# Kernel tuning notes

Measured on AMD Instinct MI355X. Metric: run time of the kernel, lower is better.

Reference implementation:

```python
import jax, jax.numpy as jnp
import numpy as np

T = 4096
VOCAB = 32000
BLANK = 0


def setup_inputs() -> dict:
    key = jax.random.key(0)
    emission = jax.random.normal(key, (T, VOCAB), dtype=jnp.float32)
    return {"emission": emission}


def reference(emission):
    """Greedy CTC decode: argmax over labels, collapse repeats, drop blanks.

    The torch module returns a variable-length Python list; for a jit-able
    fixed-shape reference we return (padded_indices, count):
      padded_indices: int32 [T], decoded labels left-packed, padded with -1
      count:          int32 scalar, number of valid labels
    """
    idx = jnp.argmax(emission, axis=-1)                      # [T] int
    # unique_consecutive: keep first element of each run
    first_of_run = jnp.concatenate(
        [jnp.array([True]), idx[1:] != idx[:-1]])            # [T] bool
    keep = first_of_run & (idx != BLANK)                     # blank filter
    # stream-compaction: left-pack kept indices, pad with -1
    pos = jnp.cumsum(keep.astype(jnp.int32)) - 1             # [T]
    dest = jnp.where(keep, pos, T)                           # T = out of bounds
    padded = jnp.full((T,), -1, dtype=jnp.int32)
    padded = padded.at[dest].set(idx.astype(jnp.int32), mode="drop")
    count = keep.sum().astype(jnp.int32)
    return padded, count
```

## Files before the change

### kernel.cpp

```cpp
#include <hip/hip_runtime.h>
#include <math.h>

#define T_STEPS 4096
#define VOCAB   32000
#define NV4     (VOCAB / 4)

__device__ __forceinline__ void comb(float& m, int& g, float om, int og) {
    if (om > m || (om == m && og < g)) { m = om; g = og; }
}

__device__ __forceinline__ void upd_group(float& m, int& g, float4 a, int j) {
    const float ma = fmaxf(fmaxf(a.x, a.y), fmaxf(a.z, a.w));
    if (ma > m) { m = ma; g = j; }
}

__global__ __launch_bounds__(256, 8) void ctc_argmax_kernel(const float* __restrict__ em,
                                                            int* __restrict__ idx_out) {
    const int t   = blockIdx.x;
    const int tid = threadIdx.x;
    const float4* row4 = (const float4*)(em + (size_t)t * VOCAB);

    float m0 = -INFINITY, m1 = -INFINITY, m2 = -INFINITY, m3 = -INFINITY;
    int   g0 = 0x7fffffff, g1 = 0x7fffffff, g2 = 0x7fffffff, g3 = 0x7fffffff;

    #pragma unroll 1
    for (int it = 0; it < 7; ++it) {
        const int j = tid + it * 1024;
        const float4 a = row4[j];
        const float4 b = row4[j + 256];
        const float4 c = row4[j + 512];
        const float4 d = row4[j + 768];
        upd_group(m0, g0, a, j);
        upd_group(m1, g1, b, j + 256);
        upd_group(m2, g2, c, j + 512);
        upd_group(m3, g3, d, j + 768);
    }
    {
        const float4 a = row4[7168 + tid];
        upd_group(m0, g0, a, 7168 + tid);
        const float4 b = row4[7424 + tid];
        upd_group(m1, g1, b, 7424 + tid);
        const float4 c = row4[7680 + tid];
        upd_group(m2, g2, c, 7680 + tid);
        if (tid < 64) {
            const float4 d = row4[7936 + tid];
            upd_group(m3, g3, d, 7936 + tid);
        }
    }

    comb(m0, g0, m1, g1);
    comb(m2, g2, m3, g3);
    comb(m0, g0, m2, g2);

    #pragma unroll
    for (int off = 32; off > 0; off >>= 1) {
        const float om = __shfl_down(m0, off, 64);
        const int   og = __shfl_down(g0, off, 64);
        comb(m0, g0, om, og);
    }

    __shared__ float sm[4];
    __shared__ int   sg[4];
    const int lane = tid & 63;
    const int wave = tid >> 6;
    if (lane == 0) { sm[wave] = m0; sg[wave] = g0; }
    __syncthreads();
    if (tid == 0) {
        #pragma unroll
        for (int w = 1; w < 4; ++w) comb(m0, g0, sm[w], sg[w]);
        const float4 win = row4[g0];
        const int c = (win.x == m0) ? 0 : (win.y == m0) ? 1 : (win.z == m0) ? 2 : 3;
        idx_out[t] = g0 * 4 + c;
    }
}

__global__ __launch_bounds__(1024) void ctc_compact_kernel(const int* __restrict__ idx,
                                                           int* __restrict__ out) {
    __shared__ int wsum[16];
    const int tid  = threadIdx.x;
    const int base = tid * 4;

    int v[4], keep[4];
    const int prev0 = (base == 0) ? -1 : idx[base - 1];
    int cnt = 0;
    #pragma unroll
    for (int k = 0; k < 4; ++k) {
        v[k] = idx[base + k];
        const int p = (k == 0) ? prev0 : v[k - 1];
        keep[k] = (v[k] != p && v[k] != 0) ? 1 : 0;
        cnt += keep[k];
    }

    const int lane = tid & 63;
    const int wave = tid >> 6;
    int incl = cnt;
    #pragma unroll
    for (int off = 1; off < 64; off <<= 1) {
        int n = __shfl_up(incl, off, 64);
        if (lane >= off) incl += n;
    }
    if (lane == 63) wsum[wave] = incl;

    #pragma unroll
    for (int k = 0; k < 4; ++k) out[base + k] = -1;
    __syncthreads();

    if (wave == 0) {
        int s = (lane < 16) ? wsum[lane] : 0;
        #pragma unroll
        for (int off = 1; off < 16; off <<= 1) {
            int n = __shfl_up(s, off, 64);
            if (lane >= off) s += n;
        }
        if (lane < 16) wsum[lane] = s;
    }
    __syncthreads();

    const int waveoff = (wave == 0) ? 0 : wsum[wave - 1];
    int pos = waveoff + incl - cnt;
    #pragma unroll
    for (int k = 0; k < 4; ++k) {
        if (keep[k]) out[pos++] = v[k];
    }
    if (tid == 0) out[T_STEPS] = wsum[15];
}

extern "C" void kernel_launch(void* const* d_in, const int* in_sizes, int n_in,
                              void* d_out, int out_size, void* d_ws, size_t ws_size,
                              hipStream_t stream) {
    const float* em  = (const float*)d_in[0];
    int*         out = (int*)d_out;
    int*         idx = (int*)d_ws;

    ctc_argmax_kernel<<<dim3(T_STEPS), dim3(256), 0, stream>>>(em, idx);
    ctc_compact_kernel<<<dim3(1), dim3(1024), 0, stream>>>(idx, out);
}
```

Baseline: 661.1 us.

## Software-pipeline argmax row loads with 8-deep nontemporal register ring

Replaces the 7-iteration loop, which held four independent max accumulators, with a fully unrolled rotating ring of eight in-flight vector loads per thread feeding a single accumulator. The loads use nontemporal hints, and the launch bounds drop from 8 to 4 blocks per SM. The aim is to keep more memory requests in flight per thread and avoid polluting the cache with streaming data. In exchange, the larger register footprint lowers occupancy, and the single accumulator creates a serial compare chain. Because the chunks are visited in increasing order, the tie-breaking still picks the lowest index.

After: 626.2 us. -5.3%, faster.

```diff
diff --git a/kernel.cpp b/kernel.cpp
--- a/kernel.cpp
+++ b/kernel.cpp
@@ -5,72 +5,67 @@
 #define VOCAB   32000
 #define NV4     (VOCAB / 4)
 
+typedef float f32x4 __attribute__((ext_vector_type(4)));
+
 __device__ __forceinline__ void comb(float& m, int& g, float om, int og) {
     if (om > m || (om == m && og < g)) { m = om; g = og; }
 }
 
-__device__ __forceinline__ void upd_group(float& m, int& g, float4 a, int j) {
+__device__ __forceinline__ void upd_group(float& m, int& g, f32x4 a, int j) {
     const float ma = fmaxf(fmaxf(a.x, a.y), fmaxf(a.z, a.w));
     if (ma > m) { m = ma; g = j; }
 }
 
-__global__ __launch_bounds__(256, 8) void ctc_argmax_kernel(const float* __restrict__ em,
+#define NT_LOAD(k) __builtin_nontemporal_load(row4 + tid + (k) * 256)
+#define STEP(vv, it, nxt)                          \
+    upd_group(m, g, vv, tid + (it) * 256);         \
+    if ((nxt) < 31) vv = NT_LOAD(nxt);
+
+__global__ __launch_bounds__(256, 4) void ctc_argmax_kernel(const float* __restrict__ em,
                                                             int* __restrict__ idx_out) {
     const int t   = blockIdx.x;
     const int tid = threadIdx.x;
-    const float4* row4 = (const float4*)(em + (size_t)t * VOCAB);
+    const f32x4* row4 = (const f32x4*)(em + (size_t)t * VOCAB);
 
-    float m0 = -INFINITY, m1 = -INFINITY, m2 = -INFINITY, m3 = -INFINITY;
-    int   g0 = 0x7fffffff, g1 = 0x7fffffff, g2 = 0x7fffffff, g3 = 0x7fffffff;
+    float m = -INFINITY;
+    int   g = 0x7fffffff;
 
-    #pragma unroll 1
-    for (int it = 0; it < 7; ++it) {
-        const int j = tid + it * 1024;
-        const float4 a = row4[j];
-        const float4 b = row4[j + 256];
-        const float4 c = row4[j + 512];
-        const float4 d = row4[j + 768];
-        upd_group(m0, g0, a, j);
-        upd_group(m1, g1, b, j + 256);
-        upd_group(m2, g2, c, j + 512);
-        upd_group(m3, g3, d, j + 768);
+    f32x4 v0 = NT_LOAD(0), v1 = NT_LOAD(1), v2 = NT_LOAD(2), v3 = NT_LOAD(3);
+    f32x4 v4 = NT_LOAD(4), v5 = NT_LOAD(5), v6 = NT_LOAD(6), v7 = NT_LOAD(7);
+
+    STEP(v0,  0,  8) STEP(v1,  1,  9) STEP(v2,  2, 10) STEP(v3,  3, 11)
+    STEP(v4,  4, 12) STEP(v5,  5, 13) STEP(v6,  6, 14) STEP(v7,  7, 15)
+    STEP(v0,  8, 16) STEP(v1,  9, 17) STEP(v2, 10, 18) STEP(v3, 11, 19)
+    STEP(v4, 12, 20) STEP(v5, 13, 21) STEP(v6, 14, 22) STEP(v7, 15, 23)
+    STEP(v0, 16, 24) STEP(v1, 17, 25) STEP(v2, 18, 26) STEP(v3, 19, 27)
+    STEP(v4, 20, 28) STEP(v5, 21, 29) STEP(v6, 22, 30) STEP(v7, 23, 31)
+    STEP(v0, 24, 99) STEP(v1, 25, 99) STEP(v2, 26, 99) STEP(v3, 27, 99)
+    STEP(v4, 28, 99) STEP(v5, 29, 99) STEP(v6, 30, 99)
+
+    if (tid < 64) {
+        const f32x4 tv = __builtin_nontemporal_load(row4 + 7936 + tid);
+        upd_group(m, g, tv, 7936 + tid);
     }
-    {
-        const float4 a = row4[7168 + tid];
-        upd_group(m0, g0, a, 7168 + tid);
-        const float4 b = row4[7424 + tid];
-        upd_group(m1, g1, b, 7424 + tid);
-        const float4 c = row4[7680 + tid];
-        upd_group(m2, g2, c, 7680 + tid);
-        if (tid < 64) {
-            const float4 d = row4[7936 + tid];
-            upd_group(m3, g3, d, 7936 + tid);
-        }
-    }
-
-    comb(m0, g0, m1, g1);
-    comb(m2, g2, m3, g3);
-    comb(m0, g0, m2, g2);
 
     #pragma unroll
     for (int off = 32; off > 0; off >>= 1) {
-        const float om = __shfl_down(m0, off, 64);
-        const int   og = __shfl_down(g0, off, 64);
-        comb(m0, g0, om, og);
+        const float om = __shfl_down(m, off, 64);
+        const int   og = __shfl_down(g, off, 64);
+        comb(m, g, om, og);
     }
 
     __shared__ float sm[4];
     __shared__ int   sg[4];
     const int lane = tid & 63;
     const int wave = tid >> 6;
-    if (lane == 0) { sm[wave] = m0; sg[wave] = g0; }
+    if (lane == 0) { sm[wave] = m; sg[wave] = g; }
     __syncthreads();
     if (tid == 0) {
         #pragma unroll
-        for (int w = 1; w < 4; ++w) comb(m0, g0, sm[w], sg[w]);
-        const float4 win = row4[g0];
-        const int c = (win.x == m0) ? 0 : (win.y == m0) ? 1 : (win.z == m0) ? 2 : 3;
-        idx_out[t] = g0 * 4 + c;
+        for (int w = 1; w < 4; ++w) comb(m, g, sm[w], sg[w]);
+        const f32x4 win = *(row4 + g);
+        const int c = (win.x == m) ? 0 : (win.y == m) ? 1 : (win.z == m) ? 2 : 3;
+        idx_out[t] = g * 4 + c;
     }
 }
 
```
